# Kernel optimization log

Measured on AMD Instinct MI355X. Metric: run time of the kernel, lower is better.

The kernel has to match this reference:

```python
import jax, jax.numpy as jnp
import numpy as np

T, N, E, B, H = 16, 20000, 320000, 16, 64
NEG_SLOPE = 0.2


def gat_conv(x, src, dst, W, att_s, att_d, bias):
    # x: [N, Fin]; W: [Fin, heads*C]; att_s/att_d: [heads, C]; bias: [heads*C]
    n = x.shape[0]
    heads, C = att_s.shape
    h = (x @ W).reshape(n, heads, C)                      # [N, heads, C]
    a_s = (h * att_s).sum(-1)                             # [N, heads]
    a_d = (h * att_d).sum(-1)                             # [N, heads]
    e = jax.nn.leaky_relu(a_s[src] + a_d[dst], NEG_SLOPE)  # [E, heads]
    e_max = jax.ops.segment_max(e, dst, num_segments=n)
    e = jnp.exp(e - e_max[dst])
    denom = jax.ops.segment_sum(e, dst, num_segments=n)
    alpha = e / (denom[dst] + 1e-16)                      # softmax over in-edges
    msg = h[src] * alpha[:, :, None]                      # [E, heads, C]
    out = jax.ops.segment_sum(msg, dst, num_segments=n)   # [N, heads, C]
    return out.reshape(n, heads * C) + bias


def encode_frame(x, ei, batch, params):
    W1, as1, ad1, b1, W2, as2, ad2, b2 = params
    loop = jnp.arange(N)
    src = jnp.concatenate([ei[0], loop])  # add self-loops (PyG default)
    dst = jnp.concatenate([ei[1], loop])
    h = jax.nn.elu(gat_conv(x, src, dst, W1, as1, ad1, b1))   # [N, 64]
    h = jax.nn.elu(gat_conv(h, src, dst, W2, as2, ad2, b2))   # [N, 64]
    sums = jax.ops.segment_sum(h, batch, num_segments=B)       # [B, 64]
    cnt = jax.ops.segment_sum(jnp.ones((N,), h.dtype), batch, num_segments=B)
    return sums / jnp.maximum(cnt, 1.0)[:, None]


def gru(x_seq, Wih, Whh, bih, bhh):
    # x_seq: [T, B, H]; torch gate order r, z, n
    def step(h, x_t):
        gx = x_t @ Wih.T + bih
        gh = h @ Whh.T + bhh
        xr, xz, xn = jnp.split(gx, 3, axis=-1)
        hr, hz, hn = jnp.split(gh, 3, axis=-1)
        r = jax.nn.sigmoid(xr + hr)
        z = jax.nn.sigmoid(xz + hz)
        n = jnp.tanh(xn + r * hn)
        h_new = (1.0 - z) * n + z * h
        return h_new, None
    h0 = jnp.zeros((x_seq.shape[1], H), x_seq.dtype)
    h_n, _ = jax.lax.scan(step, h0, x_seq)
    return h_n


def setup_inputs() -> dict:
    key = jax.random.key(0)
    ks = jax.random.split(key, 20)
    s = 0.1
    return {
        "x": jax.random.normal(ks[0], (T, N, 7), jnp.float32),
        "edge_index": jax.random.randint(ks[1], (T, 2, E), 0, N),
        "batch": jnp.sort(jax.random.randint(ks[2], (T, N), 0, B), axis=-1),
        "W1": jax.random.normal(ks[3], (7, 2 * 32), jnp.float32) * s,
        "att_src1": jax.random.normal(ks[4], (2, 32), jnp.float32) * s,
        "att_dst1": jax.random.normal(ks[5], (2, 32), jnp.float32) * s,
        "b1": jnp.zeros((64,), jnp.float32),
        "W2": jax.random.normal(ks[6], (64, 64), jnp.float32) * s,
        "att_src2": jax.random.normal(ks[7], (1, 64), jnp.float32) * s,
        "att_dst2": jax.random.normal(ks[8], (1, 64), jnp.float32) * s,
        "b2": jnp.zeros((64,), jnp.float32),
        "Wih": jax.random.normal(ks[9], (3 * H, H), jnp.float32) * s,
        "Whh": jax.random.normal(ks[10], (3 * H, H), jnp.float32) * s,
        "bih": jnp.zeros((3 * H,), jnp.float32),
        "bhh": jnp.zeros((3 * H,), jnp.float32),
        "Wc1": jax.random.normal(ks[11], (H, 32), jnp.float32) * s,
        "bc1": jnp.zeros((32,), jnp.float32),
        "Wc2": jax.random.normal(ks[12], (32, 1), jnp.float32) * s,
        "bc2": jnp.zeros((1,), jnp.float32),
    }


def reference(x, edge_index, batch, W1, att_src1, att_dst1, b1, W2, att_src2,
              att_dst2, b2, Wih, Whh, bih, bhh, Wc1, bc1, Wc2, bc2):
    gat_params = (W1, att_src1, att_dst1, b1, W2, att_src2, att_dst2, b2)
    emb = jax.vmap(lambda xf, ef, bf: encode_frame(xf, ef, bf, gat_params))(
        x, edge_index, batch)                 # [T, B, 64]
    h_n = gru(emb, Wih, Whh, bih, bhh)        # [B, 64]
    hid = jax.nn.relu(h_n @ Wc1 + bc1)        # dropout is eval-mode identity
    logits = hid @ Wc2 + bc2                  # [B, 1]
    return logits
```

## Files before the change

kernel.cpp:

```cpp
#include <hip/hip_runtime.h>
#include <math.h>

#define T_ 16
#define N_ 20000
#define E_ 320000
#define EN_ (E_ + N_)
#define B_ 16
#define RPF 32
#define RNODES (N_ / RPF)
#define SLICE_CAP 12544
#define CPB 8
#define CHUNK4 (E_ / 4 / CPB)

__device__ __forceinline__ float lrelu(float v) { return v >= 0.f ? v : 0.2f * v; }
__device__ __forceinline__ float elu(float v) { return v > 0.f ? v : expm1f(v); }
__device__ __forceinline__ float rdlane(float v, int k) {
    return __uint_as_float(__builtin_amdgcn_readlane(__float_as_uint(v), k));
}

__device__ __forceinline__ void frame_map(int bid, int* frame, int* local) {
    int blk = bid >> 3;
    *frame = (bid & 7) * 2 + (blk & 1);
    *local = blk >> 1;
}

__global__ __launch_bounds__(256) void k_h1(
    const float* __restrict__ x, const float* __restrict__ W1,
    const float* __restrict__ as1, const float* __restrict__ ad1,
    float* __restrict__ h1, float* __restrict__ a_s, float* __restrict__ a_d) {
    int lane = threadIdx.x & 63;
    int wid = (blockIdx.x * blockDim.x + threadIdx.x) >> 6;
    int nw = (gridDim.x * blockDim.x) >> 6;
    float w[7];
#pragma unroll
    for (int k = 0; k < 7; ++k) w[k] = W1[k * 64 + lane];
    float asl = as1[lane], adl = ad1[lane];
    float xv = (wid < T_ * N_ && lane < 7) ? x[(size_t)wid * 7 + lane] : 0.f;
    for (int r = wid; r < T_ * N_; r += nw) {
        float xcur = xv;
        int rn = r + nw;
        if (rn < T_ * N_ && lane < 7) xv = x[(size_t)rn * 7 + lane];
        float acc = 0.f;
#pragma unroll
        for (int k = 0; k < 7; ++k) acc = fmaf(rdlane(xcur, k), w[k], acc);
        h1[(size_t)r * 64 + lane] = acc;
        float s = acc * asl, d = acc * adl;
#pragma unroll
        for (int m = 1; m < 32; m <<= 1) { s += __shfl_xor(s, m); d += __shfl_xor(d, m); }
        if ((lane & 31) == 0) {
            a_s[r * 2 + (lane >> 5)] = s;
            a_d[r * 2 + (lane >> 5)] = d;
        }
    }
}

__global__ __launch_bounds__(256) void k_bcnt(const int* __restrict__ ei,
                                              int* __restrict__ blkCnt) {
    int t = blockIdx.x & 15, c = blockIdx.x >> 4;
    __shared__ int cl[RPF];
    if (threadIdx.x < RPF) cl[threadIdx.x] = 0;
    __syncthreads();
    const int4* db4 = (const int4*)(ei + (size_t)t * 2 * E_ + E_) + c * CHUNK4;
    for (int i = threadIdx.x; i < CHUNK4; i += 256) {
        int4 d = db4[i];
        atomicAdd(&cl[d.x / RNODES], 1);
        atomicAdd(&cl[d.y / RNODES], 1);
        atomicAdd(&cl[d.z / RNODES], 1);
        atomicAdd(&cl[d.w / RNODES], 1);
    }
    __syncthreads();
    if (threadIdx.x < RPF)
        blkCnt[(t * CPB + c) * RPF + threadIdx.x] = cl[threadIdx.x];
}

__global__ __launch_bounds__(256) void k_bscan(const int* __restrict__ blkCnt,
                                               int* __restrict__ bbase,
                                               int* __restrict__ blkOff) {
    __shared__ int a0[512], a1[512];
    int tid = threadIdx.x;
    for (int b = tid; b < 512; b += 256) {
        int t = b >> 5, rg = b & 31, s = 0;
        for (int c = 0; c < CPB; ++c) s += blkCnt[((t * CPB + c) << 5) + rg];
        a0[b] = s;
    }
    __syncthreads();
    int* src = a0; int* dst = a1;
    for (int off = 1; off < 512; off <<= 1) {
        for (int i = tid; i < 512; i += 256)
            dst[i] = src[i] + ((i >= off) ? src[i - off] : 0);
        __syncthreads();
        int* tmp = src; src = dst; dst = tmp;
    }
    if (tid == 0) bbase[0] = 0;
    for (int i = tid; i < 512; i += 256) bbase[i + 1] = src[i];
    __syncthreads();
    for (int b = tid; b < 512; b += 256) {
        int t = b >> 5, rg = b & 31;
        int run = bbase[b];
        for (int c = 0; c < CPB; ++c) {
            blkOff[((t * CPB + c) << 5) + rg] = run;
            run += blkCnt[((t * CPB + c) << 5) + rg];
        }
    }
}

__global__ __launch_bounds__(256) void k_bfill(const int* __restrict__ ei,
                                               const int* __restrict__ blkOff,
                                               int* __restrict__ bucket) {
    int t = blockIdx.x & 15, c = blockIdx.x >> 4;
    __shared__ int curL[RPF];
    if (threadIdx.x < RPF)
        curL[threadIdx.x] = blkOff[(t * CPB + c) * RPF + threadIdx.x];
    __syncthreads();
    const int4* db4 = (const int4*)(ei + (size_t)t * 2 * E_ + E_) + c * CHUNK4;
    const int4* sb4 = (const int4*)(ei + (size_t)t * 2 * E_) + c * CHUNK4;
    for (int i = threadIdx.x; i < CHUNK4; i += 256) {
        int4 d = db4[i];
        int4 s = sb4[i];
        int b, dl, p;
        b = d.x / RNODES; dl = d.x - b * RNODES;
        p = atomicAdd(&curL[b], 1); bucket[p] = (dl << 15) | s.x;
        b = d.y / RNODES; dl = d.y - b * RNODES;
        p = atomicAdd(&curL[b], 1); bucket[p] = (dl << 15) | s.y;
        b = d.z / RNODES; dl = d.z - b * RNODES;
        p = atomicAdd(&curL[b], 1); bucket[p] = (dl << 15) | s.z;
        b = d.w / RNODES; dl = d.w - b * RNODES;
        p = atomicAdd(&curL[b], 1); bucket[p] = (dl << 15) | s.w;
    }
}

__global__ __launch_bounds__(256) void k_scat2(const int* __restrict__ bucket,
                                               const int* __restrict__ bbase,
                                               int* __restrict__ rowptr,
                                               int* __restrict__ col) {
    int t = blockIdx.x & 15, rg = blockIdx.x >> 4;
    __shared__ int hist[RNODES];
    __shared__ int cur[RNODES];
    __shared__ int colL[SLICE_CAP];
    __shared__ int wsum[4];
    __shared__ int carryS;
    int tid = threadIdx.x, lane = tid & 63, wv = tid >> 6;
    int bb = bbase[t * RPF + rg];
    int cnt = bbase[t * RPF + rg + 1] - bb;
    int sliceBase = (bb - bbase[t * RPF]) + rg * RNODES;
    int r0 = rg * RNODES;
    bool ovf = (cnt + RNODES) > SLICE_CAP;
    int* rp = rowptr + t * (N_ + 1);
    int* cf = col + (size_t)t * EN_;
    for (int i = tid; i < RNODES; i += 256) hist[i] = 0;
    if (tid == 0) carryS = 0;
    __syncthreads();
    for (int i = tid; i < cnt; i += 256) atomicAdd(&hist[bucket[bb + i] >> 15], 1);
    __syncthreads();
    for (int base = 0; base < RNODES; base += 256) {
        int i = base + tid;
        int v = (i < RNODES) ? hist[i] + 1 : 0;
        int s = v;
#pragma unroll
        for (int off = 1; off < 64; off <<= 1) {
            int u = __shfl_up(s, off);
            if (lane >= off) s += u;
        }
        if (lane == 63) wsum[wv] = s;
        __syncthreads();
        if (tid == 0) {
            int a = 0;
#pragma unroll
            for (int w2 = 0; w2 < 4; ++w2) { int x2 = wsum[w2]; wsum[w2] = a; a += x2; }
        }
        __syncthreads();
        int incl = s + wsum[wv] + carryS;
        if (i < RNODES) {
            cur[i] = incl - v;
            rp[r0 + i + 1] = sliceBase + incl;
        }
        __syncthreads();
        if (tid == 255) carryS = incl;
        __syncthreads();
    }
    if (rg == 0 && tid == 0) rp[0] = 0;
    __syncthreads();
    for (int i = tid; i < cnt; i += 256) {
        int e = bucket[bb + i];
        int dl = e >> 15, src = e & 0x7FFF;
        int p = atomicAdd(&cur[dl], 1);
        if (ovf) cf[sliceBase + p] = src; else colL[p] = src;
    }
    __syncthreads();
    for (int i = tid; i < RNODES; i += 256) {
        int p = cur[i];
        if (ovf) cf[sliceBase + p] = r0 + i; else colL[p] = r0 + i;
    }
    __syncthreads();
    if (!ovf) {
        int len = cnt + RNODES;
        for (int i = tid; i < len; i += 256) cf[sliceBase + i] = colL[i];
    }
}

template <int HEADS>
__global__ __launch_bounds__(256) void k_agg(
    const int* __restrict__ rowptr, const int* __restrict__ col,
    const float* __restrict__ a_s, const float* __restrict__ a_d,
    const float* __restrict__ hin, const float* __restrict__ bias,
    float* __restrict__ outp) {
    int t, local;
    frame_map(blockIdx.x, &t, &local);
    int lane = threadIdx.x & 63;
    int n = local * 4 + (threadIdx.x >> 6);
    if (n >= N_) return;
    int node = t * N_ + n;
    float ad0 = a_d[node * HEADS];
    float ad1 = (HEADS == 2) ? a_d[node * HEADS + 1] : 0.f;
    int e0 = rowptr[t * (N_ + 1) + n], e1 = rowptr[t * (N_ + 1) + n + 1];
    const int* cb = col + (size_t)t * EN_;
    const float* hb = hin + (size_t)t * N_ * 64;
    const float* ab = a_s + (size_t)t * N_ * HEADS;
    float acc = 0.f, acc2 = 0.f, den0 = 0.f, den1 = 0.f;
    for (int base = e0; base < e1; base += 64) {
        int rem = e1 - base; if (rem > 64) rem = 64;
        int s = 0; float p0 = 0.f, p1 = 0.f;
        if (lane < rem) {
            s = cb[base + lane];
            p0 = expf(lrelu(ab[s * HEADS] + ad0));
            if (HEADS == 2) p1 = expf(lrelu(ab[s * HEADS + 1] + ad1));
        }
        den0 += p0; den1 += p1;
        int k = 0;
        for (; k + 1 < rem; k += 2) {
            int s0 = __builtin_amdgcn_readlane(s, k);
            int s1 = __builtin_amdgcn_readlane(s, k + 1);
            float pk0, pk1;
            if (HEADS == 2) {
                float pa0 = rdlane(p0, k), pa1 = rdlane(p0, k + 1);
                float pb0 = rdlane(p1, k), pb1 = rdlane(p1, k + 1);
                pk0 = (lane < 32) ? pa0 : pb0;
                pk1 = (lane < 32) ? pa1 : pb1;
            } else {
                pk0 = rdlane(p0, k); pk1 = rdlane(p0, k + 1);
            }
            acc  = fmaf(pk0, hb[(size_t)s0 * 64 + lane], acc);
            acc2 = fmaf(pk1, hb[(size_t)s1 * 64 + lane], acc2);
        }
        if (k < rem) {
            int s0 = __builtin_amdgcn_readlane(s, k);
            float pk0 = (HEADS == 2) ? ((lane < 32) ? rdlane(p0, k) : rdlane(p1, k))
                                     : rdlane(p0, k);
            acc = fmaf(pk0, hb[(size_t)s0 * 64 + lane], acc);
        }
    }
    acc += acc2;
#pragma unroll
    for (int m = 1; m < 64; m <<= 1) {
        den0 += __shfl_xor(den0, m);
        if (HEADS == 2) den1 += __shfl_xor(den1, m);
    }
    float den = (HEADS == 2) ? ((lane < 32) ? den0 : den1) : den0;
    outp[(size_t)node * 64 + lane] = elu(acc / (den + 1e-16f) + bias[lane]);
}

__global__ __launch_bounds__(256) void k_h2(
    const float* __restrict__ xin, const float* __restrict__ W2,
    const float* __restrict__ as2, const float* __restrict__ ad2,
    float* __restrict__ h2, float* __restrict__ a_s, float* __restrict__ a_d) {
    int lane = threadIdx.x & 63;
    int wid = (blockIdx.x * blockDim.x + threadIdx.x) >> 6;
    int nw = (gridDim.x * blockDim.x) >> 6;
    float w[64];
#pragma unroll
    for (int k = 0; k < 64; ++k) w[k] = W2[k * 64 + lane];
    float asl = as2[lane], adl = ad2[lane];
    float xv = (wid < T_ * N_) ? xin[(size_t)wid * 64 + lane] : 0.f;
    for (int r = wid; r < T_ * N_; r += nw) {
        float xcur = xv;
        int rn = r + nw;
        if (rn < T_ * N_) xv = xin[(size_t)rn * 64 + lane];
        float acc = 0.f;
#pragma unroll
        for (int k = 0; k < 64; ++k) acc = fmaf(rdlane(xcur, k), w[k], acc);
        h2[(size_t)r * 64 + lane] = acc;
        float s = acc * asl, d = acc * adl;
#pragma unroll
        for (int m = 1; m < 64; m <<= 1) { s += __shfl_xor(s, m); d += __shfl_xor(d, m); }
        if (lane == 0) { a_s[r] = s; a_d[r] = d; }
    }
}

__global__ void k_pool(const float* __restrict__ hact, const int* __restrict__ batch,
                       float* __restrict__ sums, float* __restrict__ cnt) {
    int wid = (blockIdx.x * blockDim.x + threadIdx.x) >> 6;
    int lane = threadIdx.x & 63;
    const int WPF = (N_ + 63) / 64;
    int t = wid / WPF, w = wid - t * WPF;
    if (t >= T_) return;
    int n0 = w * 64, n1 = min(n0 + 64, N_);
    float acc = 0.f, cacc = 0.f;
    int cur_b = batch[t * N_ + n0];
    for (int n = n0; n < n1; ++n) {
        int b = batch[t * N_ + n];
        if (b != cur_b) {
            atomicAdd(&sums[(t * B_ + cur_b) * 64 + lane], acc);
            if (lane == 0) atomicAdd(&cnt[t * B_ + cur_b], cacc);
            acc = 0.f; cacc = 0.f; cur_b = b;
        }
        acc += hact[(size_t)(t * N_ + n) * 64 + lane];
        cacc += 1.f;
    }
    atomicAdd(&sums[(t * B_ + cur_b) * 64 + lane], acc);
    if (lane == 0) atomicAdd(&cnt[t * B_ + cur_b], cacc);
}

__global__ void k_emb(const float* __restrict__ sums, const float* __restrict__ cnt,
                      float* __restrict__ emb) {
    int idx = blockIdx.x * blockDim.x + threadIdx.x;
    if (idx >= T_ * B_ * 64) return;
    emb[idx] = sums[idx] / fmaxf(cnt[idx >> 6], 1.0f);
}

__global__ void k_gx(const float* __restrict__ emb, const float* __restrict__ Wih,
                     const float* __restrict__ bih, float* __restrict__ gx) {
    int idx = blockIdx.x * blockDim.x + threadIdx.x;
    if (idx >= T_ * B_ * 192) return;
    int tb = idx / 192, g = idx - tb * 192;
    const float* er = emb + tb * 64;
    const float* wr = Wih + g * 64;
    float acc = bih[g];
#pragma unroll
    for (int k = 0; k < 64; ++k) acc = fmaf(er[k], wr[k], acc);
    gx[idx] = acc;
}

__global__ __launch_bounds__(1024) void k_gru(
    const float* __restrict__ gx_all, const float* __restrict__ Whh,
    const float* __restrict__ bhh, const float* __restrict__ Wc1,
    const float* __restrict__ bc1, const float* __restrict__ Wc2,
    const float* __restrict__ bc2, float* __restrict__ out) {
    __shared__ float Wh[192 * 65];
    __shared__ float hL[16 * 64];
    __shared__ float gh[16 * 192];
    __shared__ float hid[16 * 32];
    int tid = threadIdx.x;
    for (int i = tid; i < 192 * 64; i += 1024) Wh[(i >> 6) * 65 + (i & 63)] = Whh[i];
    hL[tid] = 0.f;
    __syncthreads();
    for (int t = 0; t < T_; ++t) {
        for (int idx = tid; idx < 16 * 192; idx += 1024) {
            int b = idx / 192, g = idx - b * 192;
            float acc = bhh[g];
            const float* wr = Wh + g * 65;
            const float* hr = hL + b * 64;
#pragma unroll
            for (int k = 0; k < 64; ++k) acc = fmaf(hr[k], wr[k], acc);
            gh[idx] = acc;
        }
        __syncthreads();
        const float* gxt = gx_all + t * 16 * 192;
        {
            int b = tid >> 6, c = tid & 63;
            float xr = gxt[b * 192 + c], xz = gxt[b * 192 + 64 + c], xn = gxt[b * 192 + 128 + c];
            float hr_ = gh[b * 192 + c], hz = gh[b * 192 + 64 + c], hn = gh[b * 192 + 128 + c];
            float r = 1.f / (1.f + expf(-(xr + hr_)));
            float z = 1.f / (1.f + expf(-(xz + hz)));
            float n = tanhf(xn + r * hn);
            hL[tid] = (1.f - z) * n + z * hL[tid];
        }
        __syncthreads();
    }
    for (int idx = tid; idx < 16 * 32; idx += 1024) {
        int b = idx >> 5, j = idx & 31;
        float acc = bc1[j];
#pragma unroll
        for (int k = 0; k < 64; ++k) acc = fmaf(hL[b * 64 + k], Wc1[k * 32 + j], acc);
        hid[idx] = fmaxf(acc, 0.f);
    }
    __syncthreads();
    if (tid < 16) {
        float acc = bc2[0];
#pragma unroll
        for (int k = 0; k < 32; ++k) acc = fmaf(hid[tid * 32 + k], Wc2[k], acc);
        out[tid] = acc;
    }
}

extern "C" void kernel_launch(void* const* d_in, const int* in_sizes, int n_in,
                              void* d_out, int out_size, void* d_ws, size_t ws_size,
                              hipStream_t stream) {
    const float* x   = (const float*)d_in[0];
    const int*   ei  = (const int*)d_in[1];
    const int* batch = (const int*)d_in[2];
    const float* W1  = (const float*)d_in[3];
    const float* as1 = (const float*)d_in[4];
    const float* ad1 = (const float*)d_in[5];
    const float* b1  = (const float*)d_in[6];
    const float* W2  = (const float*)d_in[7];
    const float* as2 = (const float*)d_in[8];
    const float* ad2 = (const float*)d_in[9];
    const float* b2  = (const float*)d_in[10];
    const float* Wih = (const float*)d_in[11];
    const float* Whh = (const float*)d_in[12];
    const float* bih = (const float*)d_in[13];
    const float* bhh = (const float*)d_in[14];
    const float* Wc1 = (const float*)d_in[15];
    const float* bc1 = (const float*)d_in[16];
    const float* Wc2 = (const float*)d_in[17];
    const float* bc2 = (const float*)d_in[18];
    float* out = (float*)d_out;

    float* ws = (float*)d_ws;
    float* hA     = ws;
    float* hX     = hA + 20480000;
    float* a_s    = hX + 20480000;
    float* a_d    = a_s + 640000;
    int*   rowptr = (int*)(a_d + 640000);
    int*   col    = rowptr + 320032;
    float* sums   = (float*)(col + 5440000);
    float* cnt    = sums + 16384;
    float* emb    = cnt + 256;
    float* gx     = emb + 16384;
    int*   blkCnt = (int*)(gx + 49152);
    int*   blkOff = blkCnt + 4096;
    int*   bbase  = blkOff + 4096;
    int*   bucket = (int*)hA;

    const int BPF_AGG = (N_ + 3) / 4;

    hipMemsetAsync(sums, 0, (size_t)(16384 + 256) * 4, stream);

    k_bcnt<<<16 * CPB, 256, 0, stream>>>(ei, blkCnt);
    k_bscan<<<1, 256, 0, stream>>>(blkCnt, bbase, blkOff);
    k_bfill<<<16 * CPB, 256, 0, stream>>>(ei, blkOff, bucket);
    k_scat2<<<16 * RPF, 256, 0, stream>>>(bucket, bbase, rowptr, col);

    k_h1<<<1024, 256, 0, stream>>>(x, W1, as1, ad1, hA, a_s, a_d);
    k_agg<2><<<16 * BPF_AGG, 256, 0, stream>>>(rowptr, col, a_s, a_d, hA, b1, hX);

    k_h2<<<1024, 256, 0, stream>>>(hX, W2, as2, ad2, hA, a_s, a_d);
    k_agg<1><<<16 * BPF_AGG, 256, 0, stream>>>(rowptr, col, a_s, a_d, hA, b2, hX);

    {
        const int WPF = (N_ + 63) / 64;
        int waves = T_ * WPF;
        k_pool<<<(waves * 64 + 255) / 256, 256, 0, stream>>>(hX, batch, sums, cnt);
    }
    k_emb<<<(T_ * B_ * 64 + 255) / 256, 256, 0, stream>>>(sums, cnt, emb);
    k_gx<<<(T_ * B_ * 192 + 255) / 256, 256, 0, stream>>>(emb, Wih, bih, gx);
    k_gru<<<1, 1024, 0, stream>>>(gx, Whh, bhh, Wc1, bc1, Wc2, bc2, out);
}
```

Baseline: 966.3 us.

## Fuse bucket count/scan/fill into one pass with fixed-capacity buckets; unroll aggregation 4x

New measurement: 871.5 us. 9.8% less time.

```diff
diff --git a/kernel.cpp b/kernel.cpp
--- a/kernel.cpp
+++ b/kernel.cpp
@@ -9,7 +9,8 @@
 #define RPF 32
 #define RNODES (N_ / RPF)
 #define SLICE_CAP 12544
-#define CPB 8
+#define BCAP 13000
+#define CPB 64
 #define CHUNK4 (E_ / 4 / CPB)
 
 __device__ __forceinline__ float lrelu(float v) { return v >= 0.f ? v : 0.2f * v; }
@@ -54,13 +55,16 @@
     }
 }
 
-__global__ __launch_bounds__(256) void k_bcnt(const int* __restrict__ ei,
-                                              int* __restrict__ blkCnt) {
+__global__ __launch_bounds__(256) void k_bfill2(const int* __restrict__ ei,
+                                                int* __restrict__ gcur,
+                                                int* __restrict__ bucket) {
     int t = blockIdx.x & 15, c = blockIdx.x >> 4;
     __shared__ int cl[RPF];
+    __shared__ int rbase[RPF];
     if (threadIdx.x < RPF) cl[threadIdx.x] = 0;
     __syncthreads();
     const int4* db4 = (const int4*)(ei + (size_t)t * 2 * E_ + E_) + c * CHUNK4;
+    const int4* sb4 = (const int4*)(ei + (size_t)t * 2 * E_) + c * CHUNK4;
     for (int i = threadIdx.x; i < CHUNK4; i += 256) {
         int4 d = db4[i];
         atomicAdd(&cl[d.x / RNODES], 1);
@@ -69,68 +73,32 @@
         atomicAdd(&cl[d.w / RNODES], 1);
     }
     __syncthreads();
-    if (threadIdx.x < RPF)
-        blkCnt[(t * CPB + c) * RPF + threadIdx.x] = cl[threadIdx.x];
-}
-
-__global__ __launch_bounds__(256) void k_bscan(const int* __restrict__ blkCnt,
-                                               int* __restrict__ bbase,
-                                               int* __restrict__ blkOff) {
-    __shared__ int a0[512], a1[512];
-    int tid = threadIdx.x;
-    for (int b = tid; b < 512; b += 256) {
-        int t = b >> 5, rg = b & 31, s = 0;
-        for (int c = 0; c < CPB; ++c) s += blkCnt[((t * CPB + c) << 5) + rg];
-        a0[b] = s;
-    }
-    __syncthreads();
-    int* src = a0; int* dst = a1;
-    for (int off = 1; off < 512; off <<= 1) {
-        for (int i = tid; i < 512; i += 256)
-            dst[i] = src[i] + ((i >= off) ? src[i - off] : 0);
-        __syncthreads();
-        int* tmp = src; src = dst; dst = tmp;
-    }
-    if (tid == 0) bbase[0] = 0;
-    for (int i = tid; i < 512; i += 256) bbase[i + 1] = src[i];
-    __syncthreads();
-    for (int b = tid; b < 512; b += 256) {
-        int t = b >> 5, rg = b & 31;
-        int run = bbase[b];
-        for (int c = 0; c < CPB; ++c) {
-            blkOff[((t * CPB + c) << 5) + rg] = run;
-            run += blkCnt[((t * CPB + c) << 5) + rg];
-        }
-    }
-}
-
-__global__ __launch_bounds__(256) void k_bfill(const int* __restrict__ ei,
-                                               const int* __restrict__ blkOff,
-                                               int* __restrict__ bucket) {
-    int t = blockIdx.x & 15, c = blockIdx.x >> 4;
-    __shared__ int curL[RPF];
-    if (threadIdx.x < RPF)
-        curL[threadIdx.x] = blkOff[(t * CPB + c) * RPF + threadIdx.x];
-    __syncthreads();
-    const int4* db4 = (const int4*)(ei + (size_t)t * 2 * E_ + E_) + c * CHUNK4;
-    const int4* sb4 = (const int4*)(ei + (size_t)t * 2 * E_) + c * CHUNK4;
+    if (threadIdx.x < RPF) {
+        rbase[threadIdx.x] = atomicAdd(&gcur[t * RPF + threadIdx.x], cl[threadIdx.x]);
+        cl[threadIdx.x] = 0;
+    }
+    __syncthreads();
     for (int i = threadIdx.x; i < CHUNK4; i += 256) {
         int4 d = db4[i];
         int4 s = sb4[i];
         int b, dl, p;
         b = d.x / RNODES; dl = d.x - b * RNODES;
-        p = atomicAdd(&curL[b], 1); bucket[p] = (dl << 15) | s.x;
+        p = rbase[b] + atomicAdd(&cl[b], 1);
+        bucket[(size_t)(t * RPF + b) * BCAP + p] = (dl << 15) | s.x;
         b = d.y / RNODES; dl = d.y - b * RNODES;
-        p = atomicAdd(&curL[b], 1); bucket[p] = (dl << 15) | s.y;
+        p = rbase[b] + atomicAdd(&cl[b], 1);
+        bucket[(size_t)(t * RPF + b) * BCAP + p] = (dl << 15) | s.y;
         b = d.z / RNODES; dl = d.z - b * RNODES;
-        p = atomicAdd(&curL[b], 1); bucket[p] = (dl << 15) | s.z;
+        p = rbase[b] + atomicAdd(&cl[b], 1);
+        bucket[(size_t)(t * RPF + b) * BCAP + p] = (dl << 15) | s.z;
         b = d.w / RNODES; dl = d.w - b * RNODES;
-        p = atomicAdd(&curL[b], 1); bucket[p] = (dl << 15) | s.w;
+        p = rbase[b] + atomicAdd(&cl[b], 1);
+        bucket[(size_t)(t * RPF + b) * BCAP + p] = (dl << 15) | s.w;
     }
 }
 
 __global__ __launch_bounds__(256) void k_scat2(const int* __restrict__ bucket,
-                                               const int* __restrict__ bbase,
+                                               const int* __restrict__ gcur,
                                                int* __restrict__ rowptr,
                                                int* __restrict__ col) {
     int t = blockIdx.x & 15, rg = blockIdx.x >> 4;
@@ -140,17 +108,25 @@
     __shared__ int wsum[4];
     __shared__ int carryS;
     int tid = threadIdx.x, lane = tid & 63, wv = tid >> 6;
-    int bb = bbase[t * RPF + rg];
-    int cnt = bbase[t * RPF + rg + 1] - bb;
-    int sliceBase = (bb - bbase[t * RPF]) + rg * RNODES;
+    int vcnt = (lane < RPF) ? gcur[t * RPF + lane] : 0;
+    int sc = vcnt;
+#pragma unroll
+    for (int off = 1; off < RPF; off <<= 1) {
+        int u = __shfl_up(sc, off);
+        if (lane >= off) sc += u;
+    }
+    int cnt = __shfl(vcnt, rg);
+    int inclAt = __shfl(sc, rg);
+    int sliceBase = (inclAt - cnt) + rg * RNODES;
     int r0 = rg * RNODES;
+    const int* bk = bucket + (size_t)(t * RPF + rg) * BCAP;
     bool ovf = (cnt + RNODES) > SLICE_CAP;
     int* rp = rowptr + t * (N_ + 1);
     int* cf = col + (size_t)t * EN_;
     for (int i = tid; i < RNODES; i += 256) hist[i] = 0;
     if (tid == 0) carryS = 0;
     __syncthreads();
-    for (int i = tid; i < cnt; i += 256) atomicAdd(&hist[bucket[bb + i] >> 15], 1);
+    for (int i = tid; i < cnt; i += 256) atomicAdd(&hist[bk[i] >> 15], 1);
     __syncthreads();
     for (int base = 0; base < RNODES; base += 256) {
         int i = base + tid;
@@ -181,7 +157,7 @@
     if (rg == 0 && tid == 0) rp[0] = 0;
     __syncthreads();
     for (int i = tid; i < cnt; i += 256) {
-        int e = bucket[bb + i];
+        int e = bk[i];
         int dl = e >> 15, src = e & 0x7FFF;
         int p = atomicAdd(&cur[dl], 1);
         if (ovf) cf[sliceBase + p] = src; else colL[p] = src;
@@ -212,44 +188,55 @@
     int node = t * N_ + n;
     float ad0 = a_d[node * HEADS];
     float ad1 = (HEADS == 2) ? a_d[node * HEADS + 1] : 0.f;
-    int e0 = rowptr[t * (N_ + 1) + n], e1 = rowptr[t * (N_ + 1) + n + 1];
+    int e0 = __builtin_amdgcn_readfirstlane(rowptr[t * (N_ + 1) + n]);
+    int e1 = __builtin_amdgcn_readfirstlane(rowptr[t * (N_ + 1) + n + 1]);
     const int* cb = col + (size_t)t * EN_;
     const float* hb = hin + (size_t)t * N_ * 64;
     const float* ab = a_s + (size_t)t * N_ * HEADS;
-    float acc = 0.f, acc2 = 0.f, den0 = 0.f, den1 = 0.f;
+    float acc0 = 0.f, acc1 = 0.f, acc2 = 0.f, acc3 = 0.f, den0 = 0.f, den1 = 0.f;
     for (int base = e0; base < e1; base += 64) {
         int rem = e1 - base; if (rem > 64) rem = 64;
         int s = 0; float p0 = 0.f, p1 = 0.f;
         if (lane < rem) {
             s = cb[base + lane];
-            p0 = expf(lrelu(ab[s * HEADS] + ad0));
-            if (HEADS == 2) p1 = expf(lrelu(ab[s * HEADS + 1] + ad1));
+            if (HEADS == 2) {
+                float2 av = *(const float2*)(ab + s * 2);
+                p0 = expf(lrelu(av.x + ad0));
+                p1 = expf(lrelu(av.y + ad1));
+            } else {
+                p0 = expf(lrelu(ab[s] + ad0));
+            }
         }
         den0 += p0; den1 += p1;
         int k = 0;
-        for (; k + 1 < rem; k += 2) {
-            int s0 = __builtin_amdgcn_readlane(s, k);
-            int s1 = __builtin_amdgcn_readlane(s, k + 1);
-            float pk0, pk1;
+        for (; k + 4 <= rem; k += 4) {
+            int sa = __builtin_amdgcn_readlane(s, k);
+            int sb = __builtin_amdgcn_readlane(s, k + 1);
+            int sc = __builtin_amdgcn_readlane(s, k + 2);
+            int sd = __builtin_amdgcn_readlane(s, k + 3);
+            float pa, pb, pc, pd;
             if (HEADS == 2) {
-                float pa0 = rdlane(p0, k), pa1 = rdlane(p0, k + 1);
-                float pb0 = rdlane(p1, k), pb1 = rdlane(p1, k + 1);
-                pk0 = (lane < 32) ? pa0 : pb0;
-                pk1 = (lane < 32) ? pa1 : pb1;
+                pa = (lane < 32) ? rdlane(p0, k) : rdlane(p1, k);
+                pb = (lane < 32) ? rdlane(p0, k + 1) : rdlane(p1, k + 1);
+                pc = (lane < 32) ? rdlane(p0, k + 2) : rdlane(p1, k + 2);
+                pd = (lane < 32) ? rdlane(p0, k + 3) : rdlane(p1, k + 3);
             } else {
-                pk0 = rdlane(p0, k); pk1 = rdlane(p0, k + 1);
+                pa = rdlane(p0, k); pb = rdlane(p0, k + 1);
+                pc = rdlane(p0, k + 2); pd = rdlane(p0, k + 3);
             }
-            acc  = fmaf(pk0, hb[(size_t)s0 * 64 + lane], acc);
-            acc2 = fmaf(pk1, hb[(size_t)s1 * 64 + lane], acc2);
-        }
-        if (k < rem) {
-            int s0 = __builtin_amdgcn_readlane(s, k);
-            float pk0 = (HEADS == 2) ? ((lane < 32) ? rdlane(p0, k) : rdlane(p1, k))
-                                     : rdlane(p0, k);
-            acc = fmaf(pk0, hb[(size_t)s0 * 64 + lane], acc);
-        }
-    }
-    acc += acc2;
+            acc0 = fmaf(pa, hb[((size_t)sa << 6) + lane], acc0);
+            acc1 = fmaf(pb, hb[((size_t)sb << 6) + lane], acc1);
+            acc2 = fmaf(pc, hb[((size_t)sc << 6) + lane], acc2);
+            acc3 = fmaf(pd, hb[((size_t)sd << 6) + lane], acc3);
+        }
+        for (; k < rem; ++k) {
+            int sa = __builtin_amdgcn_readlane(s, k);
+            float pa = (HEADS == 2) ? ((lane < 32) ? rdlane(p0, k) : rdlane(p1, k))
+                                    : rdlane(p0, k);
+            acc0 = fmaf(pa, hb[((size_t)sa << 6) + lane], acc0);
+        }
+    }
+    float acc = (acc0 + acc1) + (acc2 + acc3);
 #pragma unroll
     for (int m = 1; m < 64; m <<= 1) {
         den0 += __shfl_xor(den0, m);
@@ -417,19 +404,16 @@
     float* cnt    = sums + 16384;
     float* emb    = cnt + 256;
     float* gx     = emb + 16384;
-    int*   blkCnt = (int*)(gx + 49152);
-    int*   blkOff = blkCnt + 4096;
-    int*   bbase  = blkOff + 4096;
+    int*   gcur   = (int*)(gx + 49152);
     int*   bucket = (int*)hA;
 
     const int BPF_AGG = (N_ + 3) / 4;
 
+    hipMemsetAsync(gcur, 0, (size_t)512 * 4, stream);
     hipMemsetAsync(sums, 0, (size_t)(16384 + 256) * 4, stream);
 
-    k_bcnt<<<16 * CPB, 256, 0, stream>>>(ei, blkCnt);
-    k_bscan<<<1, 256, 0, stream>>>(blkCnt, bbase, blkOff);
-    k_bfill<<<16 * CPB, 256, 0, stream>>>(ei, blkOff, bucket);
-    k_scat2<<<16 * RPF, 256, 0, stream>>>(bucket, bbase, rowptr, col);
+    k_bfill2<<<16 * CPB, 256, 0, stream>>>(ei, gcur, bucket);
+    k_scat2<<<16 * RPF, 256, 0, stream>>>(bucket, gcur, rowptr, col);
 
     k_h1<<<1024, 256, 0, stream>>>(x, W1, as1, ad1, hA, a_s, a_d);
     k_agg<2><<<16 * BPF_AGG, 256, 0, stream>>>(rowptr, col, a_s, a_d, hA, b1, hX);
```
